# Kernel tuning notes

Measured on AMD Instinct MI355X. Metric: run time of the kernel, lower is better.

The kernel has to match this reference:

```python
import math
import jax, jax.numpy as jnp
import numpy as np

MARGIN_SCALER = 0.2
IGNORING_RATE = 0.1
NBITS = 64
TEMPERATURE = 0.1
B, L, E, D = 4096, 32, 512, 64


def setup_inputs() -> dict:
    key = jax.random.key(0)
    k1, k2, k3, k4, k5, k6 = jax.random.split(key, 6)
    return {
        "outputs_h1": jax.random.uniform(k1, (B, D), dtype=jnp.float32),
        "outputs_h2": jax.random.uniform(k2, (B, D), dtype=jnp.float32),
        "caps_embed": jax.random.normal(k3, (B, L, E), dtype=jnp.float32),
        "sim_mat": jax.random.normal(k4, (B, L, 1), dtype=jnp.float32),
        "s_v": jax.random.normal(k5, (B, D), dtype=jnp.float32),
        "s_v2": jax.random.normal(k6, (B, D), dtype=jnp.float32),
        "epochs": 5,
    }


def _cosine_sim(h, eps=1e-5):
    n = jnp.linalg.norm(h, axis=1, keepdims=True)
    a = h / jnp.maximum(n, eps)
    return a @ a.T  # [B, B]


def _self_contrastive_loss(img, tgt, caps_embed, epochs, sim_mat2d):
    batch_size = caps_embed.shape[0]
    w = jax.nn.softmax(sim_mat2d, axis=-1)              # [B, L]
    caps_mean = jnp.einsum('bl,ble->be', w, caps_embed)  # [B, E]
    cos = jnp.clip(_cosine_sim(caps_mean), 1e-6, 1.0 - 1e-6)  # [B, B]
    scores = img @ tgt.T                                 # [B, B]
    d1 = jnp.diag(scores)[:, None]
    cost_s = jnp.maximum((1.0 - cos) * MARGIN_SCALER + scores - d1, 1e-8)
    eye = jnp.eye(batch_size, dtype=cost_s.dtype)
    cost_s = cost_s * (1.0 - eye)  # masked_fill diagonal with 0
    clean_rate = epochs * IGNORING_RATE if epochs * IGNORING_RATE < 1 else 0.99
    k = math.ceil(batch_size * batch_size * (1 - clean_rate))
    thr = jnp.sort(cost_s.reshape(-1))[k - 1]  # k-th smallest (topk largest=False)
    cost_s = jnp.where(cost_s < thr, cost_s, jnp.zeros_like(cost_s))
    return cost_s.sum()


def _quantization_loss(img, nbits, lamda=1.0):
    loss = -lamda * jnp.sum((1.0 / nbits) * jnp.square(img - 0.5), axis=1)
    return loss.mean()


def _distillation_loss(stu, tcher, temperature=TEMPERATURE):
    p_t = jax.nn.log_softmax(tcher / temperature, axis=-1)
    p_s = jax.nn.log_softmax(stu / temperature, axis=-1)
    # KLDivLoss(reduction='sum', log_target=True): sum(exp(target)*(target-input))
    return jnp.sum(jnp.exp(p_t) * (p_t - p_s))


def reference(outputs_h1, outputs_h2, caps_embed, sim_mat, s_v, s_v2, epochs):
    sim2d = jax.lax.stop_gradient(sim_mat[..., 0])  # detach + squeeze(-1)
    loss1 = _self_contrastive_loss(outputs_h1, outputs_h2, caps_embed, epochs, sim2d)
    loss2 = _quantization_loss(outputs_h1, NBITS)
    loss3 = _distillation_loss(s_v2, s_v)
    # AutomaticWeightedLoss(3) with freshly-initialized params = ones(3):
    # sum_i 0.5/p_i^2 * loss_i + log(1 + p_i^2) with p_i = 1
    ln2 = jnp.log(jnp.asarray(2.0, dtype=jnp.float32))
    loss_sum = 0.5 * loss1 + ln2 + 0.5 * loss2 + ln2 + 0.5 * loss3 + ln2
    return loss_sum
```

## Files before the change

### kernel.cpp

```cpp
#include <hip/hip_runtime.h>
#include <hip/hip_bf16.h>

#define TPB 256
#define CTPB 512

using f32x4  = __attribute__((ext_vector_type(4))) float;
using bf16x8 = __attribute__((ext_vector_type(8))) short;

static constexpr int BB = 4096;

static constexpr size_t OFF_AHI  = 0;
static constexpr size_t OFF_D1   = 8388608;
static constexpr size_t OFF_H1   = OFF_D1 + 16384;
static constexpr size_t OFF_GS1  = OFF_H1 + 8192;
static constexpr size_t OFF_ST   = OFF_GS1 + 16384;
static constexpr size_t OFF_HS   = OFF_ST + 256;
static constexpr size_t HS_ONE   = (size_t)BB * 64 * 2;
static constexpr size_t ZERO_OFF = OFF_H1;
static constexpr size_t ZERO_LEN = (OFF_ST + 256) - OFF_H1;

__device__ __forceinline__ void bsplit(float x, unsigned short& h, unsigned short& l)
{
    unsigned b = __float_as_uint(x);
    unsigned r = (b + 0x7FFFu + ((b >> 16) & 1u)) >> 16;
    h = (unsigned short)r;
    float hf = __uint_as_float(r << 16);
    float lof = x - hf;
    unsigned b2 = __float_as_uint(lof);
    unsigned r2 = (b2 + 0x7FFFu + ((b2 >> 16) & 1u)) >> 16;
    l = (unsigned short)r2;
}

__device__ __forceinline__ unsigned short b2h(float x)
{
    unsigned b = __float_as_uint(x);
    return (unsigned short)((b + 0x7FFFu + ((b >> 16) & 1u)) >> 16);
}

__device__ __forceinline__ void gload16(const void* g, void* l)
{
    __builtin_amdgcn_global_load_lds((const __attribute__((address_space(1))) void*)g,
                                     (__attribute__((address_space(3))) void*)l,
                                     16, 0, 0);
}

__global__ __launch_bounds__(TPB) void zero_k(char* base)
{
    unsigned* z = (unsigned*)(base + ZERO_OFF);
    const int n = (int)(ZERO_LEN / 4);
    for (int i = blockIdx.x * TPB + threadIdx.x; i < n; i += gridDim.x * TPB) z[i] = 0u;
}

__global__ __launch_bounds__(TPB) void prep_kernel(const float* __restrict__ caps,
                                                   const float* __restrict__ sim,
                                                   unsigned short* __restrict__ ahi)
{
    const int b = blockIdx.x;
    const int tid = threadIdx.x;
    __shared__ float sm[32];
    __shared__ float w[32];
    __shared__ float red[4];
    __shared__ float nrm;
    if (tid < 32) sm[tid] = sim[b * 32 + tid];
    __syncthreads();
    if (tid < 32) {
        float m = -1e30f;
        for (int l = 0; l < 32; ++l) m = fmaxf(m, sm[l]);
        float ssum = 0.f;
        for (int l = 0; l < 32; ++l) ssum += expf(sm[l] - m);
        w[tid] = expf(sm[tid] - m) / ssum;
    }
    __syncthreads();
    const float2* cb2 = (const float2*)(caps + (size_t)b * 32 * 512);
    float cx = 0.f, cy = 0.f;
    for (int l = 0; l < 32; ++l) {
        float wl = w[l];
        float2 v = cb2[l * 256 + tid];
        cx = fmaf(wl, v.x, cx);
        cy = fmaf(wl, v.y, cy);
    }
    float ss = cx * cx + cy * cy;
    #pragma unroll
    for (int off = 32; off; off >>= 1) ss += __shfl_down(ss, off, 64);
    if ((tid & 63) == 0) red[tid >> 6] = ss;
    __syncthreads();
    if (tid == 0) nrm = sqrtf(red[0] + red[1] + red[2] + red[3]);
    __syncthreads();
    float an = fmaxf(nrm, 1e-5f);
    ahi[(size_t)b * 512 + 2 * tid]     = b2h(cx / an);
    ahi[(size_t)b * 512 + 2 * tid + 1] = b2h(cy / an);
}

__global__ __launch_bounds__(TPB) void small_k(const float* __restrict__ h1f,
                                               const float* __restrict__ h2f,
                                               unsigned short* __restrict__ h1hi,
                                               unsigned short* __restrict__ h1lo,
                                               unsigned short* __restrict__ h2hi,
                                               unsigned short* __restrict__ h2lo,
                                               float* __restrict__ d1,
                                               const float* __restrict__ sv,
                                               const float* __restrict__ sv2,
                                               double* __restrict__ L)
{
    const int row  = (blockIdx.x << 2) + (threadIdx.x >> 6);
    const int lane = threadIdx.x & 63;
    const int i    = (row << 6) + lane;
    float x1 = h1f[i], x2 = h2f[i];
    unsigned short h, l;
    bsplit(x1, h, l); h1hi[i] = h; h1lo[i] = l;
    bsplit(x2, h, l); h2hi[i] = h; h2lo[i] = l;
    float p = x1 * x2;
    #pragma unroll
    for (int m = 32; m; m >>= 1) p += __shfl_xor(p, m, 64);
    if (lane == 0) d1[row] = p;
    float xq = x1 - 0.5f;
    double s2 = (double)(xq * xq);
    #pragma unroll
    for (int m = 32; m; m >>= 1) s2 += __shfl_xor(s2, m, 64);
    float xt = sv[i] / 0.1f;
    float xs = sv2[i] / 0.1f;
    float mt = xt, ms = xs;
    #pragma unroll
    for (int m = 32; m; m >>= 1) {
        mt = fmaxf(mt, __shfl_xor(mt, m, 64));
        ms = fmaxf(ms, __shfl_xor(ms, m, 64));
    }
    float et = expf(xt - mt), es = expf(xs - ms);
    float sst = et, sss = es;
    #pragma unroll
    for (int m = 32; m; m >>= 1) { sst += __shfl_xor(sst, m, 64); sss += __shfl_xor(sss, m, 64); }
    float pt = (xt - mt) - logf(sst);
    float ps = (xs - ms) - logf(sss);
    double d3 = (double)((et / sst) * (pt - ps));
    #pragma unroll
    for (int m = 32; m; m >>= 1) d3 += __shfl_xor(d3, m, 64);
    __shared__ double r2[4], r3[4];
    if (lane == 0) { r2[threadIdx.x >> 6] = s2; r3[threadIdx.x >> 6] = d3; }
    __syncthreads();
    if (threadIdx.x == 0) {
        atomicAdd(L + 1, r2[0] + r2[1] + r2[2] + r2[3]);
        atomicAdd(L + 2, r3[0] + r3[1] + r3[2] + r3[3]);
    }
}

__global__ __launch_bounds__(CTPB, 1) void cost_pass(
    const unsigned short* __restrict__ ahi,
    const unsigned short* __restrict__ h1hi, const unsigned short* __restrict__ h1lo,
    const unsigned short* __restrict__ h2hi, const unsigned short* __restrict__ h2lo,
    const float* __restrict__ d1,
    unsigned* __restrict__ hist, double* __restrict__ gsum)
{
    __shared__ char lds_raw[131072];
    __shared__ float sD1[128];
    __shared__ unsigned lh[4096];
    __shared__ float ls[2048];
    const int tid  = threadIdx.x;
    const int lane = tid & 63;
    const int wid  = tid >> 6;
    const int wr   = wid >> 2;
    const int wc   = wid & 3;

    const int orig = (int)blockIdx.x;
    const int xcd  = orig & 7;
    const int idx  = orig >> 3;
    const int bi   = (((xcd >> 1) << 3) + (idx & 7)) << 7;
    const int bj   = (((xcd & 1) << 4) + (idx >> 3)) << 7;

    f32x4 accC[4][2], accS[4][2];
    #pragma unroll
    for (int m = 0; m < 4; ++m)
        #pragma unroll
        for (int n = 0; n < 2; ++n)
            #pragma unroll
            for (int q = 0; q < 4; ++q) { accC[m][n][q] = 0.f; accS[m][n][q] = 0.f; }

    auto STAGE = [&](int t) {
        char* d = lds_raw + ((size_t)(t & 3) << 15);
        if (t < 8) {
            const int k0b = t << 7;
            #pragma unroll
            for (int q = 0; q < 2; ++q) {
                int o    = (q << 13) + (tid << 4);
                int row  = o >> 7;
                int slot = (o >> 4) & 7;
                int sc   = (slot ^ (row & 7)) << 4;
                gload16((const char*)ahi + (size_t)(bi + row) * 1024 + k0b + sc, d + o);
                gload16((const char*)ahi + (size_t)(bj + row) * 1024 + k0b + sc, d + 16384 + o);
            }
        } else {
            const int k0b = (t - 8) << 6;
            int o    = tid << 4;
            int row  = o >> 6;
            int slot = (o >> 4) & 3;
            int sc   = (slot ^ ((row >> 1) & 3)) << 4;
            size_t ra = (size_t)(bi + row) * 128 + k0b + sc;
            size_t rb = (size_t)(bj + row) * 128 + k0b + sc;
            gload16((const char*)h1hi + ra, d + o);
            gload16((const char*)h1lo + ra, d + 8192 + o);
            gload16((const char*)h2hi + rb, d + 16384 + o);
            gload16((const char*)h2lo + rb, d + 24576 + o);
        }
    };

    STAGE(0);
    STAGE(1);
    #pragma unroll 1
    for (int t = 0; t < 10; ++t) {
        if (t < 8) STAGE(t + 2);
        __builtin_amdgcn_sched_barrier(0);
        if (t < 8)       asm volatile("s_waitcnt vmcnt(8)" ::: "memory");
        else if (t == 8) asm volatile("s_waitcnt vmcnt(4)" ::: "memory");
        else             asm volatile("s_waitcnt vmcnt(0)" ::: "memory");
        __builtin_amdgcn_s_barrier();
        const char* bufb = lds_raw + ((size_t)(t & 3) << 15);
        if (t < 8) {
            #pragma unroll
            for (int ks = 0; ks < 2; ++ks) {
                bf16x8 a_[4], b_[2];
                const int pbase = (ks << 2) + (lane >> 4);
                #pragma unroll
                for (int m = 0; m < 4; ++m) {
                    int row = wr * 64 + m * 16 + (lane & 15);
                    a_[m] = *(const bf16x8*)(bufb + row * 128 + ((pbase ^ (lane & 7)) << 4));
                }
                #pragma unroll
                for (int n = 0; n < 2; ++n) {
                    int row = wc * 32 + n * 16 + (lane & 15);
                    b_[n] = *(const bf16x8*)(bufb + 16384 + row * 128 + ((pbase ^ (lane & 7)) << 4));
                }
                __builtin_amdgcn_s_setprio(1);
                #pragma unroll
                for (int m = 0; m < 4; ++m)
                    #pragma unroll
                    for (int n = 0; n < 2; ++n)
                        accC[m][n] = __builtin_amdgcn_mfma_f32_16x16x32_bf16(a_[m], b_[n], accC[m][n], 0, 0, 0);
                __builtin_amdgcn_s_setprio(0);
            }
        } else {
            const int rdsw = (((lane >> 4) ^ ((lane >> 1) & 3)) << 4);
            bf16x8 ah[4], bh[2], bl[2];
            #pragma unroll
            for (int m = 0; m < 4; ++m)
                ah[m] = *(const bf16x8*)(bufb + (size_t)(wr * 64 + m * 16 + (lane & 15)) * 64 + rdsw);
            #pragma unroll
            for (int n = 0; n < 2; ++n) {
                bh[n] = *(const bf16x8*)(bufb + 16384 + (size_t)(wc * 32 + n * 16 + (lane & 15)) * 64 + rdsw);
                bl[n] = *(const bf16x8*)(bufb + 24576 + (size_t)(wc * 32 + n * 16 + (lane & 15)) * 64 + rdsw);
            }
            __builtin_amdgcn_s_setprio(1);
            #pragma unroll
            for (int m = 0; m < 4; ++m)
                #pragma unroll
                for (int n = 0; n < 2; ++n) {
                    accS[m][n] = __builtin_amdgcn_mfma_f32_16x16x32_bf16(ah[m], bh[n], accS[m][n], 0, 0, 0);
                    accS[m][n] = __builtin_amdgcn_mfma_f32_16x16x32_bf16(ah[m], bl[n], accS[m][n], 0, 0, 0);
                }
            __builtin_amdgcn_s_setprio(0);
            bf16x8 al[4];
            #pragma unroll
            for (int m = 0; m < 4; ++m)
                al[m] = *(const bf16x8*)(bufb + 8192 + (size_t)(wr * 64 + m * 16 + (lane & 15)) * 64 + rdsw);
            __builtin_amdgcn_s_setprio(1);
            #pragma unroll
            for (int m = 0; m < 4; ++m)
                #pragma unroll
                for (int n = 0; n < 2; ++n)
                    accS[m][n] = __builtin_amdgcn_mfma_f32_16x16x32_bf16(al[m], bh[n], accS[m][n], 0, 0, 0);
            __builtin_amdgcn_s_setprio(0);
        }
        __builtin_amdgcn_sched_barrier(0);
    }

    if (tid < 128) sD1[tid] = d1[bi + tid];
    for (int q = tid; q < 4096; q += CTPB) lh[q] = 0u;
    for (int q = tid; q < 2048; q += CTPB) ls[q] = 0.f;
    __syncthreads();
    unsigned* lhW = lh + (wid >> 2) * 2048;
    const unsigned CB = __float_as_uint(1e-8f);
    unsigned nclamp = 0;
    #pragma unroll
    for (int m = 0; m < 4; ++m) {
        #pragma unroll
        for (int r = 0; r < 4; ++r) {
            const int irow = wr * 64 + m * 16 + (lane >> 4) * 4 + r;
            const int i = bi + irow;
            const float di = sD1[irow];
            #pragma unroll
            for (int n = 0; n < 2; ++n) {
                const int j = bj + wc * 32 + n * 16 + (lane & 15);
                float cosv = fminf(fmaxf(accC[m][n][r], 1e-6f), 0.999999f);
                float v = (1.0f - cosv) * 0.2f + accS[m][n][r] - di;
                v = fmaxf(v, 1e-8f);
                if (i == j) v = 0.0f;
                unsigned bits = __float_as_uint(v);
                if (bits == CB) ++nclamp;
                else {
                    atomicAdd(&lhW[bits >> 21], 1u);
                    atomicAdd(&ls[bits >> 21], v);
                }
            }
        }
    }
    if (nclamp) {
        atomicAdd(&lhW[CB >> 21], nclamp);
        atomicAdd(&ls[CB >> 21], (float)((double)nclamp * 1e-8));
    }
    __syncthreads();
    for (int q = tid; q < 2048; q += CTPB) {
        unsigned c = lh[q] + lh[2048 + q];
        if (c) atomicAdd(&hist[q], c);
        float s = ls[q];
        if (s != 0.f) atomicAdd(&gsum[q], (double)s);
    }
}

__global__ __launch_bounds__(TPB) void scan_final(
    const unsigned* __restrict__ hist, const double* __restrict__ gsum,
    const int* __restrict__ epochs_ptr, const double* __restrict__ L,
    float* __restrict__ out)
{
    const int tid = threadIdx.x;
    __shared__ unsigned wtot[4];
    __shared__ int sbin;
    __shared__ unsigned srem;
    __shared__ double dred[4];

    int e = epochs_ptr[0];
    if (e > 1000000 || e < 0) e = (int)__int_as_float(e);
    double cr = (double)e * 0.1;
    if (!(cr < 1.0)) cr = 0.99;
    double kd = ceil(16777216.0 * (1.0 - cr));
    if (kd < 1.0) kd = 1.0;
    if (kd > 16777216.0) kd = 16777216.0;
    unsigned k = (unsigned)kd;

    unsigned local[8];
    unsigned s = 0;
    #pragma unroll
    for (int r = 0; r < 8; ++r) { unsigned v = hist[tid * 8 + r]; local[r] = v; s += v; }
    unsigned inc = s;
    #pragma unroll
    for (int d = 1; d < 64; d <<= 1) {
        unsigned n = __shfl_up(inc, (unsigned)d, 64);
        if ((tid & 63) >= d) inc += n;
    }
    if ((tid & 63) == 63) wtot[tid >> 6] = inc;
    __syncthreads();
    unsigned woff = 0;
    for (int wv = 0; wv < (tid >> 6); ++wv) woff += wtot[wv];
    unsigned excl = woff + (inc - s);
    if (k > excl && k <= excl + s) {
        unsigned rem = k - excl;
        int bin = tid * 8;
        #pragma unroll
        for (int r = 0; r < 8; ++r) {
            if (rem <= local[r]) { bin = tid * 8 + r; break; }
            rem -= local[r];
        }
        sbin = bin; srem = rem;
    }
    __syncthreads();
    const int b1 = sbin;
    double s3 = 0.0;
    for (int q = tid; q < 2048; q += TPB) if (q < b1) s3 += gsum[q];
    #pragma unroll
    for (int off = 32; off; off >>= 1) s3 += __shfl_down(s3, off, 64);
    if ((tid & 63) == 0) dred[tid >> 6] = s3;
    __syncthreads();
    if (tid == 0) {
        double S1 = dred[0] + dred[1] + dred[2] + dred[3];
        unsigned cnt = hist[b1];
        unsigned rem = srem;
        double avg = (cnt > 0) ? (gsum[b1] / (double)cnt) : 0.0;
        double loss1 = S1 + (double)(rem - 1) * avg;
        double loss2 = -L[1] / (64.0 * 4096.0);
        double loss3 = L[2];
        double total = 0.5 * loss1 + 0.5 * loss2 + 0.5 * loss3
                     + 3.0 * 0.69314718055994530942;
        float v = (float)total;
        unsigned bits = __float_as_uint(v);
        unsigned lsb = (bits >> 16) & 1u;
        unsigned h = (bits + 0x7FFFu + lsb) >> 16;
        ((unsigned*)out)[0] = (bits & 0xFFFF0000u) | (h & 0xFFFFu);
    }
}

extern "C" void kernel_launch(void* const* d_in, const int* in_sizes, int n_in,
                              void* d_out, int out_size, void* d_ws, size_t ws_size,
                              hipStream_t stream) {
    const float* h1f  = (const float*)d_in[0];
    const float* h2f  = (const float*)d_in[1];
    const float* caps = (const float*)d_in[2];
    const float* sim  = (const float*)d_in[3];
    const float* sv   = (const float*)d_in[4];
    const float* sv2  = (const float*)d_in[5];
    const int*   ep   = (const int*)d_in[6];

    char* base = (char*)d_ws;
    unsigned short* AHI  = (unsigned short*)(base + OFF_AHI);
    float*    D1   = (float*)(base + OFF_D1);
    unsigned* H1   = (unsigned*)(base + OFF_H1);
    double*   GS1  = (double*)(base + OFF_GS1);
    double*   L    = (double*)(base + OFF_ST + 32);
    unsigned short* H1HI = (unsigned short*)(base + OFF_HS);
    unsigned short* H1LO = (unsigned short*)(base + OFF_HS + HS_ONE);
    unsigned short* H2HI = (unsigned short*)(base + OFF_HS + 2 * HS_ONE);
    unsigned short* H2LO = (unsigned short*)(base + OFF_HS + 3 * HS_ONE);

    zero_k<<<8, TPB, 0, stream>>>(base);
    prep_kernel<<<4096, TPB, 0, stream>>>(caps, sim, AHI);
    small_k<<<1024, TPB, 0, stream>>>(h1f, h2f, H1HI, H1LO, H2HI, H2LO, D1, sv, sv2, L);
    cost_pass<<<1024, CTPB, 0, stream>>>(AHI, H1HI, H1LO, H2HI, H2LO, D1, H1, GS1);
    scan_final<<<1, TPB, 0, stream>>>(H1, GS1, ep, L, (float*)d_out);
}
```

Measured before the change: 183.3 us.

## Merge prep, small and zero kernels into one launch; widen LDS histograms

Three front-end kernels (workspace zeroing, caption softmax-mean prep, and per-row h1/h2 split plus loss2/loss3 partials) are fused into one launch with block-range dispatch. The loss2/loss3 double atomics are replaced by per-block partial arrays that the final scan reduces. The cost pass also reuses its GEMM staging LDS for the histograms and widens them to four count copies and two sum copies, to cut shared-atomic contention. This removes launch gaps, at the cost of an extra barrier and larger histogram zeroing.

```diff
diff --git a/kernel.cpp b/kernel.cpp
--- a/kernel.cpp
+++ b/kernel.cpp
@@ -13,11 +13,12 @@
 static constexpr size_t OFF_D1   = 8388608;
 static constexpr size_t OFF_H1   = OFF_D1 + 16384;
 static constexpr size_t OFF_GS1  = OFF_H1 + 8192;
-static constexpr size_t OFF_ST   = OFF_GS1 + 16384;
-static constexpr size_t OFF_HS   = OFF_ST + 256;
+static constexpr size_t OFF_L2P  = OFF_GS1 + 16384;
+static constexpr size_t OFF_L3P  = OFF_L2P + 8192;
+static constexpr size_t OFF_HS   = OFF_L3P + 8192;
 static constexpr size_t HS_ONE   = (size_t)BB * 64 * 2;
 static constexpr size_t ZERO_OFF = OFF_H1;
-static constexpr size_t ZERO_LEN = (OFF_ST + 256) - OFF_H1;
+static constexpr size_t ZERO_LEN = OFF_L2P - OFF_H1;
 
 __device__ __forceinline__ void bsplit(float x, unsigned short& h, unsigned short& l)
 {
@@ -44,102 +45,98 @@
                                      16, 0, 0);
 }
 
-__global__ __launch_bounds__(TPB) void zero_k(char* base)
-{
-    unsigned* z = (unsigned*)(base + ZERO_OFF);
-    const int n = (int)(ZERO_LEN / 4);
-    for (int i = blockIdx.x * TPB + threadIdx.x; i < n; i += gridDim.x * TPB) z[i] = 0u;
-}
-
-__global__ __launch_bounds__(TPB) void prep_kernel(const float* __restrict__ caps,
-                                                   const float* __restrict__ sim,
-                                                   unsigned short* __restrict__ ahi)
-{
-    const int b = blockIdx.x;
+__global__ __launch_bounds__(TPB) void front_k(
+    const float* __restrict__ caps, const float* __restrict__ sim,
+    unsigned short* __restrict__ ahi,
+    const float* __restrict__ h1f, const float* __restrict__ h2f,
+    unsigned short* __restrict__ h1hi, unsigned short* __restrict__ h1lo,
+    unsigned short* __restrict__ h2hi, unsigned short* __restrict__ h2lo,
+    float* __restrict__ d1, const float* __restrict__ sv,
+    const float* __restrict__ sv2, double* __restrict__ l2part,
+    double* __restrict__ l3part, char* __restrict__ base)
+{
+    const int blk = (int)blockIdx.x;
     const int tid = threadIdx.x;
     __shared__ float sm[32];
     __shared__ float w[32];
     __shared__ float red[4];
     __shared__ float nrm;
-    if (tid < 32) sm[tid] = sim[b * 32 + tid];
-    __syncthreads();
-    if (tid < 32) {
-        float m = -1e30f;
-        for (int l = 0; l < 32; ++l) m = fmaxf(m, sm[l]);
-        float ssum = 0.f;
-        for (int l = 0; l < 32; ++l) ssum += expf(sm[l] - m);
-        w[tid] = expf(sm[tid] - m) / ssum;
-    }
-    __syncthreads();
-    const float2* cb2 = (const float2*)(caps + (size_t)b * 32 * 512);
-    float cx = 0.f, cy = 0.f;
-    for (int l = 0; l < 32; ++l) {
-        float wl = w[l];
-        float2 v = cb2[l * 256 + tid];
-        cx = fmaf(wl, v.x, cx);
-        cy = fmaf(wl, v.y, cy);
-    }
-    float ss = cx * cx + cy * cy;
-    #pragma unroll
-    for (int off = 32; off; off >>= 1) ss += __shfl_down(ss, off, 64);
-    if ((tid & 63) == 0) red[tid >> 6] = ss;
-    __syncthreads();
-    if (tid == 0) nrm = sqrtf(red[0] + red[1] + red[2] + red[3]);
-    __syncthreads();
-    float an = fmaxf(nrm, 1e-5f);
-    ahi[(size_t)b * 512 + 2 * tid]     = b2h(cx / an);
-    ahi[(size_t)b * 512 + 2 * tid + 1] = b2h(cy / an);
-}
-
-__global__ __launch_bounds__(TPB) void small_k(const float* __restrict__ h1f,
-                                               const float* __restrict__ h2f,
-                                               unsigned short* __restrict__ h1hi,
-                                               unsigned short* __restrict__ h1lo,
-                                               unsigned short* __restrict__ h2hi,
-                                               unsigned short* __restrict__ h2lo,
-                                               float* __restrict__ d1,
-                                               const float* __restrict__ sv,
-                                               const float* __restrict__ sv2,
-                                               double* __restrict__ L)
-{
-    const int row  = (blockIdx.x << 2) + (threadIdx.x >> 6);
-    const int lane = threadIdx.x & 63;
-    const int i    = (row << 6) + lane;
-    float x1 = h1f[i], x2 = h2f[i];
-    unsigned short h, l;
-    bsplit(x1, h, l); h1hi[i] = h; h1lo[i] = l;
-    bsplit(x2, h, l); h2hi[i] = h; h2lo[i] = l;
-    float p = x1 * x2;
-    #pragma unroll
-    for (int m = 32; m; m >>= 1) p += __shfl_xor(p, m, 64);
-    if (lane == 0) d1[row] = p;
-    float xq = x1 - 0.5f;
-    double s2 = (double)(xq * xq);
-    #pragma unroll
-    for (int m = 32; m; m >>= 1) s2 += __shfl_xor(s2, m, 64);
-    float xt = sv[i] / 0.1f;
-    float xs = sv2[i] / 0.1f;
-    float mt = xt, ms = xs;
-    #pragma unroll
-    for (int m = 32; m; m >>= 1) {
-        mt = fmaxf(mt, __shfl_xor(mt, m, 64));
-        ms = fmaxf(ms, __shfl_xor(ms, m, 64));
-    }
-    float et = expf(xt - mt), es = expf(xs - ms);
-    float sst = et, sss = es;
-    #pragma unroll
-    for (int m = 32; m; m >>= 1) { sst += __shfl_xor(sst, m, 64); sss += __shfl_xor(sss, m, 64); }
-    float pt = (xt - mt) - logf(sst);
-    float ps = (xs - ms) - logf(sss);
-    double d3 = (double)((et / sst) * (pt - ps));
-    #pragma unroll
-    for (int m = 32; m; m >>= 1) d3 += __shfl_xor(d3, m, 64);
     __shared__ double r2[4], r3[4];
-    if (lane == 0) { r2[threadIdx.x >> 6] = s2; r3[threadIdx.x >> 6] = d3; }
-    __syncthreads();
-    if (threadIdx.x == 0) {
-        atomicAdd(L + 1, r2[0] + r2[1] + r2[2] + r2[3]);
-        atomicAdd(L + 2, r3[0] + r3[1] + r3[2] + r3[3]);
+
+    if (blk < 4096) {
+        const int b = blk;
+        if (tid < 32) sm[tid] = sim[b * 32 + tid];
+        __syncthreads();
+        if (tid < 32) {
+            float m = -1e30f;
+            for (int l = 0; l < 32; ++l) m = fmaxf(m, sm[l]);
+            float ssum = 0.f;
+            for (int l = 0; l < 32; ++l) ssum += expf(sm[l] - m);
+            w[tid] = expf(sm[tid] - m) / ssum;
+        }
+        __syncthreads();
+        const float2* cb2 = (const float2*)(caps + (size_t)b * 32 * 512);
+        float cx = 0.f, cy = 0.f;
+        for (int l = 0; l < 32; ++l) {
+            float wl = w[l];
+            float2 v = cb2[l * 256 + tid];
+            cx = fmaf(wl, v.x, cx);
+            cy = fmaf(wl, v.y, cy);
+        }
+        float ss = cx * cx + cy * cy;
+        #pragma unroll
+        for (int off = 32; off; off >>= 1) ss += __shfl_down(ss, off, 64);
+        if ((tid & 63) == 0) red[tid >> 6] = ss;
+        __syncthreads();
+        if (tid == 0) nrm = sqrtf(red[0] + red[1] + red[2] + red[3]);
+        __syncthreads();
+        float an = fmaxf(nrm, 1e-5f);
+        ahi[(size_t)b * 512 + 2 * tid]     = b2h(cx / an);
+        ahi[(size_t)b * 512 + 2 * tid + 1] = b2h(cy / an);
+    } else if (blk < 5120) {
+        const int pb   = blk - 4096;
+        const int row  = (pb << 2) + (tid >> 6);
+        const int lane = tid & 63;
+        const int i    = (row << 6) + lane;
+        float x1 = h1f[i], x2 = h2f[i];
+        unsigned short h, l;
+        bsplit(x1, h, l); h1hi[i] = h; h1lo[i] = l;
+        bsplit(x2, h, l); h2hi[i] = h; h2lo[i] = l;
+        float p = x1 * x2;
+        #pragma unroll
+        for (int m = 32; m; m >>= 1) p += __shfl_xor(p, m, 64);
+        if (lane == 0) d1[row] = p;
+        float xq = x1 - 0.5f;
+        double s2 = (double)(xq * xq);
+        #pragma unroll
+        for (int m = 32; m; m >>= 1) s2 += __shfl_xor(s2, m, 64);
+        float xt = sv[i] / 0.1f;
+        float xs = sv2[i] / 0.1f;
+        float mt = xt, ms = xs;
+        #pragma unroll
+        for (int m = 32; m; m >>= 1) {
+            mt = fmaxf(mt, __shfl_xor(mt, m, 64));
+            ms = fmaxf(ms, __shfl_xor(ms, m, 64));
+        }
+        float et = expf(xt - mt), es = expf(xs - ms);
+        float sst = et, sss = es;
+        #pragma unroll
+        for (int m = 32; m; m >>= 1) { sst += __shfl_xor(sst, m, 64); sss += __shfl_xor(sss, m, 64); }
+        float pt = (xt - mt) - logf(sst);
+        float ps = (xs - ms) - logf(sss);
+        double d3 = (double)((et / sst) * (pt - ps));
+        #pragma unroll
+        for (int m = 32; m; m >>= 1) d3 += __shfl_xor(d3, m, 64);
+        if (lane == 0) { r2[tid >> 6] = s2; r3[tid >> 6] = d3; }
+        __syncthreads();
+        if (tid == 0) {
+            l2part[pb] = r2[0] + r2[1] + r2[2] + r2[3];
+            l3part[pb] = r3[0] + r3[1] + r3[2] + r3[3];
+        }
+    } else {
+        unsigned* z = (unsigned*)(base + ZERO_OFF);
+        const int n = (int)(ZERO_LEN / 4);
+        for (int i2 = (blk - 5120) * TPB + tid; i2 < n; i2 += 8 * TPB) z[i2] = 0u;
     }
 }
 
@@ -152,8 +149,6 @@
 {
     __shared__ char lds_raw[131072];
     __shared__ float sD1[128];
-    __shared__ unsigned lh[4096];
-    __shared__ float ls[2048];
     const int tid  = threadIdx.x;
     const int lane = tid & 63;
     const int wid  = tid >> 6;
@@ -271,11 +266,15 @@
         __builtin_amdgcn_sched_barrier(0);
     }
 
+    __syncthreads();
+    unsigned* lh = (unsigned*)lds_raw;
+    float*    ls = (float*)(lds_raw + 32768);
     if (tid < 128) sD1[tid] = d1[bi + tid];
-    for (int q = tid; q < 4096; q += CTPB) lh[q] = 0u;
-    for (int q = tid; q < 2048; q += CTPB) ls[q] = 0.f;
-    __syncthreads();
-    unsigned* lhW = lh + (wid >> 2) * 2048;
+    for (int q = tid; q < 8192; q += CTPB) lh[q] = 0u;
+    for (int q = tid; q < 4096; q += CTPB) ls[q] = 0.f;
+    __syncthreads();
+    unsigned* lhW = lh + (wid >> 1) * 2048;
+    float*    lsW = ls + (wid >> 2) * 2048;
     const unsigned CB = __float_as_uint(1e-8f);
     unsigned nclamp = 0;
     #pragma unroll
@@ -296,34 +295,34 @@
                 if (bits == CB) ++nclamp;
                 else {
                     atomicAdd(&lhW[bits >> 21], 1u);
-                    atomicAdd(&ls[bits >> 21], v);
+                    atomicAdd(&lsW[bits >> 21], v);
                 }
             }
         }
     }
     if (nclamp) {
         atomicAdd(&lhW[CB >> 21], nclamp);
-        atomicAdd(&ls[CB >> 21], (float)((double)nclamp * 1e-8));
+        atomicAdd(&lsW[CB >> 21], (float)((double)nclamp * 1e-8));
     }
     __syncthreads();
     for (int q = tid; q < 2048; q += CTPB) {
-        unsigned c = lh[q] + lh[2048 + q];
+        unsigned c = lh[q] + lh[2048 + q] + lh[4096 + q] + lh[6144 + q];
         if (c) atomicAdd(&hist[q], c);
-        float s = ls[q];
+        float s = ls[q] + ls[2048 + q];
         if (s != 0.f) atomicAdd(&gsum[q], (double)s);
     }
 }
 
 __global__ __launch_bounds__(TPB) void scan_final(
     const unsigned* __restrict__ hist, const double* __restrict__ gsum,
-    const int* __restrict__ epochs_ptr, const double* __restrict__ L,
-    float* __restrict__ out)
+    const int* __restrict__ epochs_ptr, const double* __restrict__ l2part,
+    const double* __restrict__ l3part, float* __restrict__ out)
 {
     const int tid = threadIdx.x;
     __shared__ unsigned wtot[4];
     __shared__ int sbin;
     __shared__ unsigned srem;
-    __shared__ double dred[4];
+    __shared__ double dred[4], dred2[4], dred3[4];
 
     int e = epochs_ptr[0];
     if (e > 1000000 || e < 0) e = (int)__int_as_float(e);
@@ -361,20 +360,27 @@
     }
     __syncthreads();
     const int b1 = sbin;
-    double s3 = 0.0;
+    double s3 = 0.0, p2 = 0.0, p3 = 0.0;
     for (int q = tid; q < 2048; q += TPB) if (q < b1) s3 += gsum[q];
+    for (int q = tid; q < 1024; q += TPB) { p2 += l2part[q]; p3 += l3part[q]; }
     #pragma unroll
-    for (int off = 32; off; off >>= 1) s3 += __shfl_down(s3, off, 64);
-    if ((tid & 63) == 0) dred[tid >> 6] = s3;
+    for (int off = 32; off; off >>= 1) {
+        s3 += __shfl_down(s3, off, 64);
+        p2 += __shfl_down(p2, off, 64);
+        p3 += __shfl_down(p3, off, 64);
+    }
+    if ((tid & 63) == 0) { dred[tid >> 6] = s3; dred2[tid >> 6] = p2; dred3[tid >> 6] = p3; }
     __syncthreads();
     if (tid == 0) {
         double S1 = dred[0] + dred[1] + dred[2] + dred[3];
+        double sum2 = dred2[0] + dred2[1] + dred2[2] + dred2[3];
+        double sum3 = dred3[0] + dred3[1] + dred3[2] + dred3[3];
         unsigned cnt = hist[b1];
         unsigned rem = srem;
         double avg = (cnt > 0) ? (gsum[b1] / (double)cnt) : 0.0;
         double loss1 = S1 + (double)(rem - 1) * avg;
-        double loss2 = -L[1] / (64.0 * 4096.0);
-        double loss3 = L[2];
+        double loss2 = -sum2 / (64.0 * 4096.0);
+        double loss3 = sum3;
         double total = 0.5 * loss1 + 0.5 * loss2 + 0.5 * loss3
                      + 3.0 * 0.69314718055994530942;
         float v = (float)total;
@@ -401,15 +407,16 @@
     float*    D1   = (float*)(base + OFF_D1);
     unsigned* H1   = (unsigned*)(base + OFF_H1);
     double*   GS1  = (double*)(base + OFF_GS1);
-    double*   L    = (double*)(base + OFF_ST + 32);
+    double*   L2P  = (double*)(base + OFF_L2P);
+    double*   L3P  = (double*)(base + OFF_L3P);
     unsigned short* H1HI = (unsigned short*)(base + OFF_HS);
     unsigned short* H1LO = (unsigned short*)(base + OFF_HS + HS_ONE);
     unsigned short* H2HI = (unsigned short*)(base + OFF_HS + 2 * HS_ONE);
     unsigned short* H2LO = (unsigned short*)(base + OFF_HS + 3 * HS_ONE);
 
-    zero_k<<<8, TPB, 0, stream>>>(base);
-    prep_kernel<<<4096, TPB, 0, stream>>>(caps, sim, AHI);
-    small_k<<<1024, TPB, 0, stream>>>(h1f, h2f, H1HI, H1LO, H2HI, H2LO, D1, sv, sv2, L);
+    front_k<<<5128, TPB, 0, stream>>>(caps, sim, AHI, h1f, h2f,
+                                      H1HI, H1LO, H2HI, H2LO, D1, sv, sv2,
+                                      L2P, L3P, base);
     cost_pass<<<1024, CTPB, 0, stream>>>(AHI, H1HI, H1LO, H2HI, H2LO, D1, H1, GS1);
-    scan_final<<<1, TPB, 0, stream>>>(H1, GS1, ep, L, (float*)d_out);
-}
+    scan_final<<<1, TPB, 0, stream>>>(H1, GS1, ep, L2P, L3P, (float*)d_out);
+}
```

After: 151.2 us, median of 2. 1.21x faster.
